# Kernel optimization log

Hardware: AMD Instinct MI355X
Metric: run time of the kernel (lower is better)

The kernel has to match this reference:

```python
import jax, jax.numpy as jnp
import numpy as np

N_NODES = 50000
N_EDGES = 800000
IN_F, E_F, OUT_F = 128, 32, 128

def setup_inputs() -> dict:
    key = jax.random.key(0)
    ks = jax.random.split(key, 8)
    return {
        "h": jax.random.normal(ks[0], (N_NODES, IN_F), dtype=jnp.float32),
        "eftr": jax.random.normal(ks[1], (N_EDGES, E_F), dtype=jnp.float32),
        "weight": jax.random.normal(ks[2], (IN_F + E_F, OUT_F), dtype=jnp.float32) * (1.0 / np.sqrt(IN_F + E_F)),
        "W_w": jax.random.normal(ks[3], (OUT_F, IN_F + OUT_F), dtype=jnp.float32) * (1.0 / np.sqrt(IN_F + OUT_F)),
        "W_b": jax.random.normal(ks[4], (OUT_F,), dtype=jnp.float32) * 0.01,
        "bias": jnp.zeros((OUT_F,), dtype=jnp.float32),
        "src_idx": jax.random.randint(ks[5], (N_EDGES,), 0, N_NODES, dtype=jnp.int64) if jax.config.jax_enable_x64 else jax.random.randint(ks[5], (N_EDGES,), 0, N_NODES, dtype=jnp.int32),
        "dst_idx": jax.random.randint(ks[6], (N_EDGES,), 0, N_NODES, dtype=jnp.int32),
        "num_dst": N_NODES,
    }

def reference(h, eftr, weight, W_w, W_b, bias, src_idx, dst_idx, num_dst):
    # Segment-mean of concat([h[src], eftr]) over dst neighborhoods.
    # Sum node part and edge part separately (avoids materializing the concat mailbox).
    sum_h = jax.ops.segment_sum(h[src_idx], dst_idx, num_segments=num_dst)   # [D, IN_F]
    sum_e = jax.ops.segment_sum(eftr, dst_idx, num_segments=num_dst)        # [D, E_F]
    cnt = jax.ops.segment_sum(jnp.ones((dst_idx.shape[0],), h.dtype), dst_idx, num_segments=num_dst)
    denom = jnp.maximum(cnt, 1.0)[:, None]  # zero-degree nodes -> h_neigh = 0
    feat_mean = jnp.concatenate([sum_h / denom, sum_e / denom], axis=-1)    # [D, IN_F+E_F]
    h_neigh = feat_mean @ weight                                            # [D, OUT_F]
    h_dst = h[:num_dst]
    h_prime = jnp.concatenate([h_dst, h_neigh], axis=1) @ W_w.T + W_b       # Linear W
    h_prime = h_prime + bias
    return h_prime
```

## Files before the change

### kernel.cpp

```cpp
#include <hip/hip_runtime.h>

#define NN   50000
#define NE   800000
#define INF  128
#define EF   32
#define OUTF 128
#define KDIM 288
#define NBLK ((NN + 1023) / 1024)

typedef __attribute__((ext_vector_type(8))) short     short8;
typedef __attribute__((ext_vector_type(8))) unsigned short ushort8;
typedef __attribute__((ext_vector_type(4))) float     float4v;

__device__ __forceinline__ unsigned short f2bf(float f) {
    union { float f; unsigned int u; } c; c.f = f;
    const unsigned int r = (c.u + 0x7FFFu + ((c.u >> 16) & 1u)) >> 16;
    return (unsigned short)r;
}

__global__ void prep_kernel(const float* __restrict__ weight,
                            const float* __restrict__ W_w,
                            const float* __restrict__ W_b,
                            const float* __restrict__ bias,
                            float* __restrict__ Mmat,
                            float* __restrict__ cvec) {
    __shared__ float wrow[OUTF];
    const int r = blockIdx.x;
    const int j = threadIdx.x;
    if (r < 128) {
        Mmat[r * OUTF + j] = W_w[j * 256 + r];
        return;
    }
    if (r == KDIM) {
        cvec[j] = W_b[j] + bias[j];
        return;
    }
    const int m = r - 128;
    wrow[j] = weight[m * OUTF + j];
    __syncthreads();
    float acc = 0.f;
#pragma unroll 8
    for (int k = 0; k < OUTF; ++k)
        acc += wrow[k] * W_w[j * 256 + 128 + k];
    Mmat[r * OUTF + j] = acc;
}

__global__ void pack_kernel(const float* __restrict__ Mmat,
                            unsigned short* __restrict__ Mb) {
    const int b = blockIdx.x;
    const int kb = b >> 3;
    const int ct = b & 7;
    const int lane = threadIdx.x;
    const int col = ct * 16 + (lane & 15);
    const int k0 = kb * 32 + (lane >> 4) * 8;
    ushort8 v;
#pragma unroll
    for (int i = 0; i < 8; ++i)
        v[i] = f2bf(Mmat[(size_t)(k0 + i) * OUTF + col]);
    *(ushort8*)(Mb + ((size_t)(b * 64 + lane) * 8)) = v;
}

__global__ __launch_bounds__(256)
void hist_kernel(const int* __restrict__ dst, int* __restrict__ off) {
    const int e = blockIdx.x * 256 + threadIdx.x;
    if (e < NE) atomicAdd(&off[dst[e]], 1);
}

__global__ __launch_bounds__(256)
void scan1_kernel(const int* __restrict__ off, int* __restrict__ partial) {
    const int b = blockIdx.x;
    const int tid = threadIdx.x;
    const int idx = b * 1024 + tid * 4;
    int v0 = 0, v1 = 0, v2 = 0, v3 = 0;
    if (idx + 3 < NN) {
        const int4 q = *(const int4*)(off + idx);
        v0 = q.x; v1 = q.y; v2 = q.z; v3 = q.w;
    } else {
        if (idx + 0 < NN) v0 = off[idx + 0];
        if (idx + 1 < NN) v1 = off[idx + 1];
        if (idx + 2 < NN) v2 = off[idx + 2];
    }
    int t = v0 + v1 + v2 + v3;
#pragma unroll
    for (int ofs = 32; ofs > 0; ofs >>= 1) t += __shfl_down(t, ofs);
    __shared__ int wsum[4];
    if ((tid & 63) == 0) wsum[tid >> 6] = t;
    __syncthreads();
    if (tid == 0) partial[b] = wsum[0] + wsum[1] + wsum[2] + wsum[3];
}

__global__ __launch_bounds__(256)
void scan3_kernel(int* __restrict__ off, const int* __restrict__ partial) {
    __shared__ int blockbase;
    __shared__ int wsum[4];
    const int b = blockIdx.x;
    const int tid = threadIdx.x;
    const int lane = tid & 63;
    const int wid = tid >> 6;

    if (wid == 0) {
        const int v = (lane < NBLK) ? partial[lane] : 0;
        int x = v;
#pragma unroll
        for (int ofs = 1; ofs < 64; ofs <<= 1) {
            const int t = __shfl_up(x, ofs);
            if (lane >= ofs) x += t;
        }
        if (lane == b) blockbase = x - v;
    }

    const int idx = b * 1024 + tid * 4;
    int v0 = 0, v1 = 0, v2 = 0, v3 = 0;
    if (idx + 3 < NN) {
        const int4 q = *(const int4*)(off + idx);
        v0 = q.x; v1 = q.y; v2 = q.z; v3 = q.w;
    } else {
        if (idx + 0 < NN) v0 = off[idx + 0];
        if (idx + 1 < NN) v1 = off[idx + 1];
        if (idx + 2 < NN) v2 = off[idx + 2];
    }
    const int tsum = v0 + v1 + v2 + v3;
    int x = tsum;
#pragma unroll
    for (int ofs = 1; ofs < 64; ofs <<= 1) {
        const int t = __shfl_up(x, ofs);
        if (lane >= ofs) x += t;
    }
    if (lane == 63) wsum[wid] = x;
    __syncthreads();
    int wp = 0;
    for (int w = 0; w < wid; ++w) wp += wsum[w];
    const int base = blockbase + wp + (x - tsum);
    if (idx + 0 < NN) off[idx + 0] = base;
    if (idx + 1 < NN) off[idx + 1] = base + v0;
    if (idx + 2 < NN) off[idx + 2] = base + v0 + v1;
    if (idx + 3 < NN) off[idx + 3] = base + v0 + v1 + v2;
}

__global__ __launch_bounds__(256)
void scatter_ids_kernel(const int* __restrict__ srcv,
                        const int* __restrict__ dst,
                        int* __restrict__ off,
                        int2* __restrict__ eo2) {
    const int e = blockIdx.x * 256 + threadIdx.x;
    if (e < NE) {
        const int d = dst[e];
        const int pos = atomicAdd(&off[d], 1);
        eo2[pos] = make_int2(srcv[e], e);
    }
}

__global__ __launch_bounds__(256)
void gather_kernel(const float* __restrict__ h,
                   const float* __restrict__ eftr,
                   const int* __restrict__ off,
                   const int2* __restrict__ eo2,
                   float* __restrict__ mean_h,
                   float* __restrict__ mean_e) {
    const int tid = threadIdx.x;
    const int lane = tid & 63;
    const int node = blockIdx.x * 4 + (tid >> 6);
    if (node >= NN) return;

    const int end = off[node];
    const int start = (node == 0) ? 0 : off[node - 1];

    float ax = 0.f, ay = 0.f, ae = 0.f;
    const float* hcol = h + lane * 2;
    const int el = lane & 31;
    const bool lowhalf = (lane < 32);

    for (int base = start; base < end; base += 64) {
        const int m = min(64, end - base);
        int px = 0, py = 0;
        if (base + lane < end) {
            const long long pv =
                __builtin_nontemporal_load((const long long*)(eo2 + base + lane));
            px = (int)pv;
            py = (int)(pv >> 32);
        }
        int j = 0;
        for (; j + 7 < m; j += 8) {
            int s[8], e[8];
#pragma unroll
            for (int u = 0; u < 8; ++u) {
                s[u] = __builtin_amdgcn_readlane(px, j + u);
                e[u] = __builtin_amdgcn_readlane(py, j + u);
            }
            float2 v[8];
#pragma unroll
            for (int u = 0; u < 8; ++u)
                v[u] = *(const float2*)(hcol + (size_t)s[u] * INF);
            float f[4];
#pragma unroll
            for (int u = 0; u < 4; ++u) {
                const int ee = lowhalf ? e[2 * u] : e[2 * u + 1];
                f[u] = __builtin_nontemporal_load(&eftr[(size_t)ee * EF + el]);
            }
#pragma unroll
            for (int u = 0; u < 8; ++u) { ax += v[u].x; ay += v[u].y; }
            ae += (f[0] + f[1]) + (f[2] + f[3]);
        }
        for (; j < m; ++j) {
            const int s0 = __builtin_amdgcn_readlane(px, j);
            const int e0 = __builtin_amdgcn_readlane(py, j);
            const float2 v0 = *(const float2*)(hcol + (size_t)s0 * INF);
            ax += v0.x;
            ay += v0.y;
            if (lowhalf) ae += __builtin_nontemporal_load(&eftr[(size_t)e0 * EF + el]);
        }
    }

    ae += __shfl(ae, lane + 32);

    const float inv = 1.f / fmaxf((float)(end - start), 1.f);
    *(float2*)(mean_h + (size_t)node * INF + lane * 2) =
        make_float2(ax * inv, ay * inv);
    if (lowhalf) mean_e[(size_t)node * EF + el] = ae * inv;
}

__global__ __launch_bounds__(256)
void node_gemm_kernel(const float* __restrict__ h,
                      const float* __restrict__ mean_h,
                      const float* __restrict__ mean_e,
                      const unsigned short* __restrict__ Mb,
                      const float* __restrict__ cvec,
                      float* __restrict__ out) {
    const int tid = threadIdx.x;
    const int lane = tid & 63;
    const int wid = tid >> 6;
    const int nt = blockIdx.x * 4 + wid;
    const int m16 = lane & 15;
    const int quad = lane >> 4;
    const int koff = quad * 8;

    const int anode = nt * 16 + m16;
    const int nclamp = (anode < NN) ? anode : (NN - 1);

    float4v acc[8] = {};

    for (int kb = 0; kb < 9; ++kb) {
        const float* srcp;
        if (kb < 4)
            srcp = h + (size_t)nclamp * INF + kb * 32 + koff;
        else if (kb < 8)
            srcp = mean_h + (size_t)nclamp * INF + (kb - 4) * 32 + koff;
        else
            srcp = mean_e + (size_t)nclamp * EF + koff;
        const float4 p0 = *(const float4*)srcp;
        const float4 p1 = *(const float4*)(srcp + 4);
        short8 a;
        a[0] = (short)f2bf(p0.x); a[1] = (short)f2bf(p0.y);
        a[2] = (short)f2bf(p0.z); a[3] = (short)f2bf(p0.w);
        a[4] = (short)f2bf(p1.x); a[5] = (short)f2bf(p1.y);
        a[6] = (short)f2bf(p1.z); a[7] = (short)f2bf(p1.w);

        const short8* bp = (const short8*)(Mb + (size_t)kb * 8 * 64 * 8);
#pragma unroll
        for (int ct = 0; ct < 8; ++ct) {
            const short8 b = bp[ct * 64 + lane];
            acc[ct] = __builtin_amdgcn_mfma_f32_16x16x32_bf16(a, b, acc[ct], 0, 0, 0);
        }
    }

    float cv[8];
#pragma unroll
    for (int ct = 0; ct < 8; ++ct) cv[ct] = cvec[ct * 16 + m16];

#pragma unroll
    for (int r = 0; r < 4; ++r) {
        const int nrow = nt * 16 + quad * 4 + r;
        if (nrow < NN) {
            float* orow = out + (size_t)nrow * OUTF;
#pragma unroll
            for (int ct = 0; ct < 8; ++ct)
                orow[ct * 16 + m16] = acc[ct][r] + cv[ct];
        }
    }
}

extern "C" void kernel_launch(void* const* d_in, const int* in_sizes, int n_in,
                              void* d_out, int out_size, void* d_ws, size_t ws_size,
                              hipStream_t stream) {
    const float* h      = (const float*)d_in[0];
    const float* eftr   = (const float*)d_in[1];
    const float* weight = (const float*)d_in[2];
    const float* W_w    = (const float*)d_in[3];
    const float* W_b    = (const float*)d_in[4];
    const float* bias   = (const float*)d_in[5];
    const int*   src    = (const int*)d_in[6];
    const int*   dst    = (const int*)d_in[7];
    float* out = (float*)d_out;

    float* ws      = (float*)d_ws;
    float* mean_h  = ws;
    float* mean_e  = mean_h + (size_t)NN * INF;
    float* Mmat    = mean_e + (size_t)NN * EF;
    float* cvec    = Mmat + (size_t)KDIM * OUTF;
    unsigned short* Mb = (unsigned short*)(cvec + OUTF);
    int*   off     = (int*)((char*)Mb + (size_t)9 * 8 * 64 * 8 * 2);
    int2*  eo2     = (int2*)(off + NN);
    int*   partial = (int*)(eo2 + NE);

    hipMemsetAsync(off, 0, (size_t)NN * sizeof(int), stream);

    prep_kernel<<<KDIM + 1, 128, 0, stream>>>(weight, W_w, W_b, bias, Mmat, cvec);
    pack_kernel<<<72, 64, 0, stream>>>(Mmat, Mb);
    hist_kernel<<<(NE + 255) / 256, 256, 0, stream>>>(dst, off);
    scan1_kernel<<<NBLK, 256, 0, stream>>>(off, partial);
    scan3_kernel<<<NBLK, 256, 0, stream>>>(off, partial);
    scatter_ids_kernel<<<(NE + 255) / 256, 256, 0, stream>>>(src, dst, off, eo2);
    gather_kernel<<<(NN + 3) / 4, 256, 0, stream>>>(h, eftr, off, eo2,
                                                    mean_h, mean_e);
    node_gemm_kernel<<<(NN / 64) + 1, 256, 0, stream>>>(h, mean_h, mean_e,
                                                        Mb, cvec, out);
}
```

Baseline: 340.9 us.

## Gather bf16 node features and store bf16 means for the GEMM

A new kernel converts h to bf16 once. The gather then reads 4-byte bf16 pairs instead of float2, halving the random-access traffic for neighbor features, and writes bf16 means that the GEMM loads directly without converting. The histogram and scatter kernels also now process four edges per thread using int4 loads. The cost is one extra conversion pass over h and some added rounding, since the inputs are quantized to bf16 before summation rather than after.

```diff
diff --git a/kernel.cpp b/kernel.cpp
--- a/kernel.cpp
+++ b/kernel.cpp
@@ -61,9 +61,26 @@
 }
 
 __global__ __launch_bounds__(256)
+void cvt_h_kernel(const float* __restrict__ h, unsigned short* __restrict__ hb) {
+    const size_t i = (size_t)(blockIdx.x * 256 + threadIdx.x) * 8;
+    const float4 a = *(const float4*)(h + i);
+    const float4 b = *(const float4*)(h + i + 4);
+    ushort8 v;
+    v[0] = f2bf(a.x); v[1] = f2bf(a.y); v[2] = f2bf(a.z); v[3] = f2bf(a.w);
+    v[4] = f2bf(b.x); v[5] = f2bf(b.y); v[6] = f2bf(b.z); v[7] = f2bf(b.w);
+    *(ushort8*)(hb + i) = v;
+}
+
+__global__ __launch_bounds__(256)
 void hist_kernel(const int* __restrict__ dst, int* __restrict__ off) {
-    const int e = blockIdx.x * 256 + threadIdx.x;
-    if (e < NE) atomicAdd(&off[dst[e]], 1);
+    const int e = (blockIdx.x * 256 + threadIdx.x) * 4;
+    if (e < NE) {
+        const int4 d = *(const int4*)(dst + e);
+        atomicAdd(&off[d.x], 1);
+        atomicAdd(&off[d.y], 1);
+        atomicAdd(&off[d.z], 1);
+        atomicAdd(&off[d.w], 1);
+    }
 }
 
 __global__ __launch_bounds__(256)
@@ -142,21 +159,25 @@
                         const int* __restrict__ dst,
                         int* __restrict__ off,
                         int2* __restrict__ eo2) {
-    const int e = blockIdx.x * 256 + threadIdx.x;
+    const int e = (blockIdx.x * 256 + threadIdx.x) * 4;
     if (e < NE) {
-        const int d = dst[e];
-        const int pos = atomicAdd(&off[d], 1);
-        eo2[pos] = make_int2(srcv[e], e);
-    }
-}
-
-__global__ __launch_bounds__(256)
-void gather_kernel(const float* __restrict__ h,
+        const int4 s = *(const int4*)(srcv + e);
+        const int4 d = *(const int4*)(dst + e);
+        int p;
+        p = atomicAdd(&off[d.x], 1); eo2[p] = make_int2(s.x, e + 0);
+        p = atomicAdd(&off[d.y], 1); eo2[p] = make_int2(s.y, e + 1);
+        p = atomicAdd(&off[d.z], 1); eo2[p] = make_int2(s.z, e + 2);
+        p = atomicAdd(&off[d.w], 1); eo2[p] = make_int2(s.w, e + 3);
+    }
+}
+
+__global__ __launch_bounds__(256)
+void gather_kernel(const unsigned short* __restrict__ hb,
                    const float* __restrict__ eftr,
                    const int* __restrict__ off,
                    const int2* __restrict__ eo2,
-                   float* __restrict__ mean_h,
-                   float* __restrict__ mean_e) {
+                   unsigned short* __restrict__ mean_h,
+                   unsigned short* __restrict__ mean_e) {
     const int tid = threadIdx.x;
     const int lane = tid & 63;
     const int node = blockIdx.x * 4 + (tid >> 6);
@@ -166,7 +187,7 @@
     const int start = (node == 0) ? 0 : off[node - 1];
 
     float ax = 0.f, ay = 0.f, ae = 0.f;
-    const float* hcol = h + lane * 2;
+    const unsigned short* hcol = hb + lane * 2;
     const int el = lane & 31;
     const bool lowhalf = (lane < 32);
 
@@ -187,10 +208,10 @@
                 s[u] = __builtin_amdgcn_readlane(px, j + u);
                 e[u] = __builtin_amdgcn_readlane(py, j + u);
             }
-            float2 v[8];
+            unsigned v[8];
 #pragma unroll
             for (int u = 0; u < 8; ++u)
-                v[u] = *(const float2*)(hcol + (size_t)s[u] * INF);
+                v[u] = *(const unsigned*)(hcol + (size_t)s[u] * INF);
             float f[4];
 #pragma unroll
             for (int u = 0; u < 4; ++u) {
@@ -198,15 +219,22 @@
                 f[u] = __builtin_nontemporal_load(&eftr[(size_t)ee * EF + el]);
             }
 #pragma unroll
-            for (int u = 0; u < 8; ++u) { ax += v[u].x; ay += v[u].y; }
+            for (int u = 0; u < 8; ++u) {
+                union { unsigned u; float f; } lo, hi;
+                lo.u = v[u] << 16;
+                hi.u = v[u] & 0xffff0000u;
+                ax += lo.f; ay += hi.f;
+            }
             ae += (f[0] + f[1]) + (f[2] + f[3]);
         }
         for (; j < m; ++j) {
             const int s0 = __builtin_amdgcn_readlane(px, j);
             const int e0 = __builtin_amdgcn_readlane(py, j);
-            const float2 v0 = *(const float2*)(hcol + (size_t)s0 * INF);
-            ax += v0.x;
-            ay += v0.y;
+            const unsigned v0 = *(const unsigned*)(hcol + (size_t)s0 * INF);
+            union { unsigned u; float f; } lo, hi;
+            lo.u = v0 << 16;
+            hi.u = v0 & 0xffff0000u;
+            ax += lo.f; ay += hi.f;
             if (lowhalf) ae += __builtin_nontemporal_load(&eftr[(size_t)e0 * EF + el]);
         }
     }
@@ -214,15 +242,16 @@
     ae += __shfl(ae, lane + 32);
 
     const float inv = 1.f / fmaxf((float)(end - start), 1.f);
-    *(float2*)(mean_h + (size_t)node * INF + lane * 2) =
-        make_float2(ax * inv, ay * inv);
-    if (lowhalf) mean_e[(size_t)node * EF + el] = ae * inv;
-}
-
-__global__ __launch_bounds__(256)
-void node_gemm_kernel(const float* __restrict__ h,
-                      const float* __restrict__ mean_h,
-                      const float* __restrict__ mean_e,
+    const unsigned mx = f2bf(ax * inv);
+    const unsigned my = f2bf(ay * inv);
+    *(unsigned*)(mean_h + (size_t)node * INF + lane * 2) = mx | (my << 16);
+    if (lowhalf) mean_e[(size_t)node * EF + el] = f2bf(ae * inv);
+}
+
+__global__ __launch_bounds__(256)
+void node_gemm_kernel(const unsigned short* __restrict__ hb,
+                      const unsigned short* __restrict__ mean_h,
+                      const unsigned short* __restrict__ mean_e,
                       const unsigned short* __restrict__ Mb,
                       const float* __restrict__ cvec,
                       float* __restrict__ out) {
@@ -240,20 +269,14 @@
     float4v acc[8] = {};
 
     for (int kb = 0; kb < 9; ++kb) {
-        const float* srcp;
+        const unsigned short* srcp;
         if (kb < 4)
-            srcp = h + (size_t)nclamp * INF + kb * 32 + koff;
+            srcp = hb + (size_t)nclamp * INF + kb * 32 + koff;
         else if (kb < 8)
             srcp = mean_h + (size_t)nclamp * INF + (kb - 4) * 32 + koff;
         else
             srcp = mean_e + (size_t)nclamp * EF + koff;
-        const float4 p0 = *(const float4*)srcp;
-        const float4 p1 = *(const float4*)(srcp + 4);
-        short8 a;
-        a[0] = (short)f2bf(p0.x); a[1] = (short)f2bf(p0.y);
-        a[2] = (short)f2bf(p0.z); a[3] = (short)f2bf(p0.w);
-        a[4] = (short)f2bf(p1.x); a[5] = (short)f2bf(p1.y);
-        a[6] = (short)f2bf(p1.z); a[7] = (short)f2bf(p1.w);
+        const short8 a = *(const short8*)(const void*)srcp;
 
         const short8* bp = (const short8*)(Mb + (size_t)kb * 8 * 64 * 8);
 #pragma unroll
@@ -292,26 +315,28 @@
     const int*   dst    = (const int*)d_in[7];
     float* out = (float*)d_out;
 
-    float* ws      = (float*)d_ws;
-    float* mean_h  = ws;
-    float* mean_e  = mean_h + (size_t)NN * INF;
-    float* Mmat    = mean_e + (size_t)NN * EF;
-    float* cvec    = Mmat + (size_t)KDIM * OUTF;
-    unsigned short* Mb = (unsigned short*)(cvec + OUTF);
-    int*   off     = (int*)((char*)Mb + (size_t)9 * 8 * 64 * 8 * 2);
-    int2*  eo2     = (int2*)(off + NN);
-    int*   partial = (int*)(eo2 + NE);
+    char* base = (char*)d_ws;
+    unsigned short* mean_h = (unsigned short*)(base);
+    unsigned short* mean_e = (unsigned short*)(base + 12800000);
+    unsigned short* h_bf   = (unsigned short*)(base + 16000000);
+    float* Mmat            = (float*)(base + 28800000);
+    float* cvec            = (float*)(base + 28947456);
+    unsigned short* Mb     = (unsigned short*)(base + 28947968);
+    int*   off             = (int*)(base + 29021696);
+    int2*  eo2             = (int2*)(base + 29221696);
+    int*   partial         = (int*)(base + 35621696);
 
     hipMemsetAsync(off, 0, (size_t)NN * sizeof(int), stream);
 
     prep_kernel<<<KDIM + 1, 128, 0, stream>>>(weight, W_w, W_b, bias, Mmat, cvec);
     pack_kernel<<<72, 64, 0, stream>>>(Mmat, Mb);
-    hist_kernel<<<(NE + 255) / 256, 256, 0, stream>>>(dst, off);
+    cvt_h_kernel<<<3125, 256, 0, stream>>>(h, h_bf);
+    hist_kernel<<<(NE / 4 + 255) / 256, 256, 0, stream>>>(dst, off);
     scan1_kernel<<<NBLK, 256, 0, stream>>>(off, partial);
     scan3_kernel<<<NBLK, 256, 0, stream>>>(off, partial);
-    scatter_ids_kernel<<<(NE + 255) / 256, 256, 0, stream>>>(src, dst, off, eo2);
-    gather_kernel<<<(NN + 3) / 4, 256, 0, stream>>>(h, eftr, off, eo2,
+    scatter_ids_kernel<<<(NE / 4 + 255) / 256, 256, 0, stream>>>(src, dst, off, eo2);
+    gather_kernel<<<(NN + 3) / 4, 256, 0, stream>>>(h_bf, eftr, off, eo2,
                                                     mean_h, mean_e);
-    node_gemm_kernel<<<(NN / 64) + 1, 256, 0, stream>>>(h, mean_h, mean_e,
+    node_gemm_kernel<<<(NN / 64) + 1, 256, 0, stream>>>(h_bf, mean_h, mean_e,
                                                         Mb, cvec, out);
 }
```

New measurement: 325.6 us. 1.05x faster.
